# Kernel optimization log

Hardware: AMD Instinct MI355X
Metric: run time of the kernel (lower is better)

## Reference

```python
import jax, jax.numpy as jnp
import numpy as np

B = 256          # batch
H = 1024         # conditioning_size (dec_hid_dim)
D = 256          # gst_dim
G = 32           # num_gst
C = 16           # num_cells
O = 256          # output_size


def setup_inputs() -> dict:
    key = jax.random.key(0)
    ks = jax.random.split(key, 7)
    hidden = jax.random.normal(ks[0], (B, H), dtype=jnp.float32)
    # per-cell embedding tables: nn.Embedding(num_gst, gst_dim) stacked over cells
    gst_emb = jax.random.normal(ks[1], (C, G, D), dtype=jnp.float32)
    # per-cell Linear(gst_dim + cond, cond): weight [H, H + D] (torch [out, in]), bias [H]
    attn_w = jax.random.normal(ks[2], (C, H, H + D), dtype=jnp.float32) * 0.02
    attn_b = jax.random.normal(ks[3], (C, H), dtype=jnp.float32) * 0.02
    # per-cell v: Parameter(torch.rand(cond))
    v = jax.random.uniform(ks[4], (C, H), dtype=jnp.float32)
    # out Linear(gst_dim, output_size)
    out_w = jax.random.normal(ks[5], (O, D), dtype=jnp.float32) * 0.02
    out_b = jax.random.normal(ks[6], (O,), dtype=jnp.float32) * 0.02
    return {"hidden": hidden, "gst_emb": gst_emb, "attn_w": attn_w,
            "attn_b": attn_b, "v": v, "out_w": out_w, "out_b": out_b}


def reference(hidden, gst_emb, attn_w, attn_b, v, out_w, out_b):
    # Original concatenates (hidden, encoder_outputs) along features; split the
    # linear weight accordingly instead of materializing the concat.
    w_hid = attn_w[:, :, :H]        # [C, H, H]
    w_enc = attn_w[:, :, H:]        # [C, H, D]
    # embedding lookup of arange(G) == the table rows themselves (same for all batch)
    enc = gst_emb                   # [C, G, D]
    hid_part = jnp.einsum('bh,coh->bco', hidden, w_hid)     # [B, C, Ho]
    enc_part = jnp.einsum('cgd,cod->cgo', enc, w_enc)       # [C, G, Ho]
    energy = jnp.tanh(hid_part[:, :, None, :] + enc_part[None]
                      + attn_b[None, :, None, :])           # [B, C, G, Ho]
    scores = jnp.einsum('bcgh,ch->bcg', energy, v)          # [B, C, G]
    attention = jax.nn.softmax(scores, axis=-1)             # softmax over num_gst
    weighted = jnp.einsum('bcg,cgd->bcd', attention, enc)   # [B, C, D]
    att_cat = attention.reshape(B, C * G)                   # torch.cat(att_list, dim=1)
    pooled = jnp.mean(weighted, axis=1)                     # [B, D]
    out = pooled @ out_w.T + out_b                          # [B, O]
    return (att_cat, out)
```

## Files before the change

### kernel.cpp

```cpp
#include <hip/hip_runtime.h>
#include <hip/hip_bf16.h>

#define B_  256
#define H_  1024
#define D_  256
#define G_  32
#define C_  16
#define O_  256
#define HD_ 1280
#define N1_ 16384
#define RS_ 40

typedef __attribute__((ext_vector_type(8)))  short short8;
typedef __attribute__((ext_vector_type(4)))  short s16x4;
typedef __attribute__((ext_vector_type(4)))  float f32x4;
typedef __attribute__((ext_vector_type(16))) float f32x16;

#define MFMA32(a, b, c) __builtin_amdgcn_mfma_f32_32x32x16_bf16((a), (b), (c), 0, 0, 0)

__device__ __forceinline__ float tanh_c(float x) {
    float y = __expf(2.f * x);
    float t = 1.f - 2.f * __builtin_amdgcn_rcpf(y + 1.f);
    return fminf(fmaxf(t, -0.99999994f), 0.99999994f);
}

__device__ __forceinline__ short bfhi(float x) {
    return (short)(__float_as_uint(x) >> 16);
}
__device__ __forceinline__ short bflo(float x) {
    float fhi = __uint_as_float(__float_as_uint(x) & 0xFFFF0000u);
    return (short)(__float_as_uint(x - fhi) >> 16);
}

__device__ __forceinline__ void split4(const float4 v, s16x4& hi, s16x4& lo) {
    hi[0] = bfhi(v.x); lo[0] = bflo(v.x);
    hi[1] = bfhi(v.y); lo[1] = bflo(v.y);
    hi[2] = bfhi(v.z); lo[2] = bflo(v.z);
    hi[3] = bfhi(v.w); lo[3] = bflo(v.w);
}

__global__ __launch_bounds__(256, 2) void gemm1_kernel(
    const short* __restrict__ hidH, const short* __restrict__ hidL,
    const float* __restrict__ attn_w, const float* __restrict__ attn_b,
    float* __restrict__ hp)
{
    __shared__ short BsH[2][32 * RS_];
    __shared__ short BsL[2][32 * RS_];

    const int tid  = threadIdx.x;
    const int wave = tid >> 6, lane = tid & 63;
    const int n0  = blockIdx.x * 32;
    const int l31 = lane & 31;
    const int kh  = (lane >> 5) * 8;

    f32x16 acc0, acc1;
    #pragma unroll
    for (int i = 0; i < 16; ++i) { acc0[i] = 0.f; acc1[i] = 0.f; }

    const int rB = tid >> 3, cB = (tid & 7) * 4;
    const float* pB = attn_w + (size_t)(n0 + rB) * HD_ + cB;
    const int wB = rB * RS_ + cB;
    const int boff = l31 * RS_ + kh;

    const size_t aBase = (size_t)(wave * 2) * 32768 + (size_t)lane * 8;
    const short* pH0 = hidH + aBase;
    const short* pH1 = hidH + aBase + 32768;
    const short* pL0 = hidL + aBase;
    const short* pL1 = hidL + aBase + 32768;

    float4 rb[2];
    short8 aH0[2][2], aH1[2][2], aL0[2][2], aL1[2][2];

    rb[0] = *(const float4*)(pB);
    {   s16x4 h_, l_; split4(rb[0], h_, l_);
        *(s16x4*)(&BsH[0][wB]) = h_;
        *(s16x4*)(&BsL[0][wB]) = l_; }
    rb[1] = *(const float4*)(pB + 32);
    aH0[0][0] = *(const short8*)(pH0);
    aH0[0][1] = *(const short8*)(pH0 + 512);
    aH1[0][0] = *(const short8*)(pH1);
    aH1[0][1] = *(const short8*)(pH1 + 512);
    aL0[0][0] = *(const short8*)(pL0);
    aL0[0][1] = *(const short8*)(pL0 + 512);
    aL1[0][0] = *(const short8*)(pL1);
    aL1[0][1] = *(const short8*)(pL1 + 512);
    asm volatile("s_waitcnt lgkmcnt(0)" ::: "memory");
    __builtin_amdgcn_s_barrier();

#define BODY(P, K0, DOW, DOLB, DOLA, DOB)                                     \
    {                                                                         \
        if (DOW) {                                                            \
            s16x4 h_, l_;                                                     \
            split4(rb[P ^ 1], h_, l_);                                        \
            *(s16x4*)(&BsH[P ^ 1][wB]) = h_;                                  \
            *(s16x4*)(&BsL[P ^ 1][wB]) = l_;                                  \
        }                                                                     \
        if (DOLB) rb[P] = *(const float4*)(pB + ((K0) + 2) * 32);             \
        if (DOLA) {                                                           \
            aH0[P ^ 1][0] = *(const short8*)(pH0 + ((K0) + 1) * 1024);        \
            aH0[P ^ 1][1] = *(const short8*)(pH0 + ((K0) + 1) * 1024 + 512);  \
            aH1[P ^ 1][0] = *(const short8*)(pH1 + ((K0) + 1) * 1024);        \
            aH1[P ^ 1][1] = *(const short8*)(pH1 + ((K0) + 1) * 1024 + 512);  \
            aL0[P ^ 1][0] = *(const short8*)(pL0 + ((K0) + 1) * 1024);        \
            aL0[P ^ 1][1] = *(const short8*)(pL0 + ((K0) + 1) * 1024 + 512);  \
            aL1[P ^ 1][0] = *(const short8*)(pL1 + ((K0) + 1) * 1024);        \
            aL1[P ^ 1][1] = *(const short8*)(pL1 + ((K0) + 1) * 1024 + 512);  \
        }                                                                     \
        {                                                                     \
            short8 bh0 = *(const short8*)(&BsH[P][boff]);                     \
            short8 bl0 = *(const short8*)(&BsL[P][boff]);                     \
            short8 bh1 = *(const short8*)(&BsH[P][boff + 16]);                \
            short8 bl1 = *(const short8*)(&BsL[P][boff + 16]);                \
            __builtin_amdgcn_s_setprio(1);                                    \
            acc0 = MFMA32(aH0[P][0], bh0, acc0);                              \
            acc1 = MFMA32(aH1[P][0], bh0, acc1);                              \
            acc0 = MFMA32(aL0[P][0], bh0, acc0);                              \
            acc1 = MFMA32(aL1[P][0], bh0, acc1);                              \
            acc0 = MFMA32(aH0[P][0], bl0, acc0);                              \
            acc1 = MFMA32(aH1[P][0], bl0, acc1);                              \
            acc0 = MFMA32(aH0[P][1], bh1, acc0);                              \
            acc1 = MFMA32(aH1[P][1], bh1, acc1);                              \
            acc0 = MFMA32(aL0[P][1], bh1, acc0);                              \
            acc1 = MFMA32(aL1[P][1], bh1, acc1);                              \
            acc0 = MFMA32(aH0[P][1], bl1, acc0);                              \
            acc1 = MFMA32(aH1[P][1], bl1, acc1);                              \
            __builtin_amdgcn_s_setprio(0);                                    \
        }                                                                     \
        if (DOB) {                                                            \
            asm volatile("s_waitcnt lgkmcnt(0)" ::: "memory");                \
            __builtin_amdgcn_s_barrier();                                     \
        }                                                                     \
    }

    for (int k0 = 0; k0 < 30; k0 += 2) {
        BODY(0, k0, 1, 1, 1, 1)
        BODY(1, k0 + 1, 1, 1, 1, 1)
    }
    BODY(0, 30, 1, 0, 1, 1)
    BODY(1, 31, 0, 0, 0, 0)
#undef BODY

    const int col  = n0 + l31;
    const float bias = attn_b[col];
    const int rbase = wave * 64 + (lane >> 5) * 4;
    float* dcol = hp + col;
    #pragma unroll
    for (int r = 0; r < 16; ++r) {
        const int row = rbase + (r & 3) + 8 * (r >> 2);
        dcol[(size_t)row * N1_]        = tanh_c(acc0[r] + bias);
        dcol[(size_t)(row + 32) * N1_] = tanh_c(acc1[r] + bias);
    }
}

__global__ __launch_bounds__(256) void gemm2_kernel(
    const float* __restrict__ enc, const float* __restrict__ attn_w,
    const float* __restrict__ hidden, float* __restrict__ ep,
    short* __restrict__ hidH, short* __restrict__ hidL)
{
    const int tid  = threadIdx.x;
    const int wave = tid >> 6, lane = tid & 63;

    {
        const int bid = blockIdx.y * 16 + blockIdx.x;
        const int gid = bid * 256 + tid;
        if (gid < 32768) {
            const int s   = gid >> 12;
            const int k0  = (gid >> 7) & 31;
            const int ks  = (gid >> 6) & 1;
            const int ln  = gid & 63;
            const int row = s * 32 + (ln & 31);
            const int colk = k0 * 32 + ks * 16 + (ln >> 5) * 8;
            const float* src = hidden + (size_t)row * H_ + colk;
            s16x4 h0, l0, h1, l1;
            split4(*(const float4*)src, h0, l0);
            split4(*(const float4*)(src + 4), h1, l1);
            *(short8*)(hidH + (size_t)gid * 8) =
                short8{h0[0],h0[1],h0[2],h0[3],h1[0],h1[1],h1[2],h1[3]};
            *(short8*)(hidL + (size_t)gid * 8) =
                short8{l0[0],l0[1],l0[2],l0[3],l1[0],l1[1],l1[2],l1[3]};
        }
    }

    const int c  = blockIdx.y;
    const int n0 = blockIdx.x * 64 + wave * 16;
    const int l16 = lane & 15;
    const int lk  = (lane >> 4) * 8;

#define MFMA16(a, b, c) __builtin_amdgcn_mfma_f32_16x16x32_bf16((a), (b), (c), 0, 0, 0)
    f32x4 acc[2];
    acc[0] = f32x4{0.f, 0.f, 0.f, 0.f};
    acc[1] = f32x4{0.f, 0.f, 0.f, 0.f};

    const float* encp = enc + c * (G_ * D_);
    const float* wp   = attn_w + (size_t)c * H_ * HD_ + H_;

    #pragma unroll
    for (int kk = 0; kk < 8; ++kk) {
        const int k0 = kk * 32 + lk;
        short8 ah[2], al[2], bh, bl;
        #pragma unroll
        for (int mi = 0; mi < 2; ++mi) {
            const float* p = encp + (mi * 16 + l16) * D_ + k0;
            s16x4 h0, l0, h1, l1;
            split4(*(const float4*)p, h0, l0);
            split4(*(const float4*)(p + 4), h1, l1);
            ah[mi] = short8{h0[0],h0[1],h0[2],h0[3],h1[0],h1[1],h1[2],h1[3]};
            al[mi] = short8{l0[0],l0[1],l0[2],l0[3],l1[0],l1[1],l1[2],l1[3]};
        }
        {
            const float* p = wp + (size_t)(n0 + l16) * HD_ + k0;
            s16x4 h0, l0, h1, l1;
            split4(*(const float4*)p, h0, l0);
            split4(*(const float4*)(p + 4), h1, l1);
            bh = short8{h0[0],h0[1],h0[2],h0[3],h1[0],h1[1],h1[2],h1[3]};
            bl = short8{l0[0],l0[1],l0[2],l0[3],l1[0],l1[1],l1[2],l1[3]};
        }
        #pragma unroll
        for (int mi = 0; mi < 2; ++mi) {
            acc[mi] = MFMA16(ah[mi], bh, acc[mi]);
            acc[mi] = MFMA16(al[mi], bh, acc[mi]);
            acc[mi] = MFMA16(ah[mi], bl, acc[mi]);
        }
    }

    const int lr = (lane >> 4) * 4;
    #pragma unroll
    for (int mi = 0; mi < 2; ++mi) {
        const int g = mi * 16 + lr;
        const int o = n0 + l16;
        float* dst = ep + (c * G_ + g) * H_ + o;
        f32x4 vacc = acc[mi];
        dst[0]      = tanh_c(vacc[0]);
        dst[H_]     = tanh_c(vacc[1]);
        dst[2 * H_] = tanh_c(vacc[2]);
        dst[3 * H_] = tanh_c(vacc[3]);
    }
#undef MFMA16
}

__global__ __launch_bounds__(256) void attn_kernel(
    const float* __restrict__ hp, const float* __restrict__ ep,
    const float* __restrict__ v, const float* __restrict__ enc,
    float* __restrict__ out, float* __restrict__ wt)
{
    const int c  = blockIdx.x;
    const int b0 = blockIdx.y * 4;
    const int tid  = threadIdx.x;
    const int wave = tid >> 6, lane = tid & 63;

    __shared__ float s_att[4][G_];
    __shared__ float s_sc[4][G_];

    f32x4 vv[4], tav[4][4];
    const float* vrow = v + c * H_;
    #pragma unroll
    for (int j = 0; j < 4; ++j)
        vv[j] = *(const f32x4*)(vrow + lane * 4 + j * 256);
    #pragma unroll
    for (int bi = 0; bi < 4; ++bi) {
        const float* hprow = hp + (size_t)(b0 + bi) * N1_ + c * H_;
        #pragma unroll
        for (int j = 0; j < 4; ++j)
            tav[bi][j] = *(const f32x4*)(hprow + lane * 4 + j * 256);
    }

    #pragma unroll
    for (int gg = 0; gg < 8; ++gg) {
        const int g = wave * 8 + gg;
        const float* eprow = ep + (size_t)(c * G_ + g) * H_;
        float s[4] = {0.f, 0.f, 0.f, 0.f};
        #pragma unroll
        for (int j = 0; j < 4; ++j) {
            const f32x4 tb = *(const f32x4*)(eprow + lane * 4 + j * 256);
            #pragma unroll
            for (int e = 0; e < 4; ++e) {
                const float tbx = tb[e];
                const float w   = vv[j][e];
                #pragma unroll
                for (int bi = 0; bi < 4; ++bi) {
                    const float ta  = tav[bi][j][e];
                    const float num = ta + tbx;
                    const float den = fmaf(ta, tbx, 1.f);
                    s[bi] = fmaf(num * __builtin_amdgcn_rcpf(den), w, s[bi]);
                }
            }
        }
        #pragma unroll
        for (int off = 32; off > 0; off >>= 1) {
            s[0] += __shfl_down(s[0], off, 64);
            s[1] += __shfl_down(s[1], off, 64);
            s[2] += __shfl_down(s[2], off, 64);
            s[3] += __shfl_down(s[3], off, 64);
        }
        if (lane == 0) {
            s_sc[0][g] = s[0]; s_sc[1][g] = s[1];
            s_sc[2][g] = s[2]; s_sc[3][g] = s[3];
        }
    }
    __syncthreads();

    if (tid < 128) {
        const int bi = tid >> 5, g = tid & 31;
        float sv = s_sc[bi][g];
        float m = sv;
        #pragma unroll
        for (int off = 16; off > 0; off >>= 1)
            m = fmaxf(m, __shfl_xor(m, off, 32));
        const float e = __expf(sv - m);
        float sum = e;
        #pragma unroll
        for (int off = 16; off > 0; off >>= 1)
            sum += __shfl_xor(sum, off, 32);
        const float a = e / sum;
        s_att[bi][g] = a;
        out[(size_t)(b0 + bi) * (C_ * G_) + c * G_ + g] = a;
    }
    __syncthreads();

    float w0 = 0.f, w1 = 0.f, w2 = 0.f, w3 = 0.f;
    const float* encc = enc + c * (G_ * D_) + tid;
    #pragma unroll
    for (int g = 0; g < G_; ++g) {
        const float e = encc[g * D_];
        w0 = fmaf(s_att[0][g], e, w0);
        w1 = fmaf(s_att[1][g], e, w1);
        w2 = fmaf(s_att[2][g], e, w2);
        w3 = fmaf(s_att[3][g], e, w3);
    }
    wt[(size_t)((b0 + 0) * C_ + c) * D_ + tid] = w0;
    wt[(size_t)((b0 + 1) * C_ + c) * D_ + tid] = w1;
    wt[(size_t)((b0 + 2) * C_ + c) * D_ + tid] = w2;
    wt[(size_t)((b0 + 3) * C_ + c) * D_ + tid] = w3;
}

__global__ __launch_bounds__(256) void out_kernel(
    const float* __restrict__ wt, const float* __restrict__ out_w,
    const float* __restrict__ out_b, float* __restrict__ out)
{
    const int b = blockIdx.x, tid = threadIdx.x;
    __shared__ float pooled[D_];

    float s = 0.f;
    #pragma unroll
    for (int c = 0; c < C_; ++c)
        s += wt[(size_t)(b * C_ + c) * D_ + tid];
    pooled[tid] = s * (1.f / 16.f);
    __syncthreads();

    float acc = out_b[tid];
    const float* wrow = out_w + tid * D_;
    #pragma unroll 8
    for (int dc = 0; dc < 64; ++dc) {
        float4 w4 = *(const float4*)(wrow + dc * 4);
        acc += pooled[dc * 4 + 0] * w4.x;
        acc += pooled[dc * 4 + 1] * w4.y;
        acc += pooled[dc * 4 + 2] * w4.z;
        acc += pooled[dc * 4 + 3] * w4.w;
    }
    out[(size_t)B_ * (C_ * G_) + b * O_ + tid] = acc;
}

extern "C" void kernel_launch(void* const* d_in, const int* in_sizes, int n_in,
                              void* d_out, int out_size, void* d_ws, size_t ws_size,
                              hipStream_t stream) {
    const float* hidden = (const float*)d_in[0];
    const float* enc    = (const float*)d_in[1];
    const float* attn_w = (const float*)d_in[2];
    const float* attn_b = (const float*)d_in[3];
    const float* v      = (const float*)d_in[4];
    const float* out_w  = (const float*)d_in[5];
    const float* out_b  = (const float*)d_in[6];
    float* out = (float*)d_out;

    float* hp = (float*)d_ws;
    float* ep = hp + (size_t)B_ * N1_;
    float* wt = ep + (size_t)C_ * G_ * H_;
    short* hidH = (short*)(wt + (size_t)B_ * C_ * D_);
    short* hidL = hidH + (size_t)B_ * H_;

    gemm2_kernel<<<dim3(16, C_), 256, 0, stream>>>(enc, attn_w, hidden, ep, hidH, hidL);
    gemm1_kernel<<<512, 256, 0, stream>>>(hidH, hidL, attn_w, attn_b, hp);
    attn_kernel<<<dim3(C_, B_ / 4), 256, 0, stream>>>(hp, ep, v, enc, out, wt);
    out_kernel<<<B_, 256, 0, stream>>>(wt, out_w, out_b, out);
}
```

Before: 205.4 us.

## Load GEMM1 weight fragments directly into registers, dropping LDS staging and barriers

The hidden-projection GEMM no longer stages the fp32 attention weights through shared memory with per-step barriers. Each wave now loads its own weight fragment from global memory into registers, splits it into bf16 hi/lo, and uses a three-deep register prefetch pipeline for both operands. The grid is remapped so each block covers 64 output columns and 4 batch slabs, with each wave owning a 32-column by 64-row tile. This removes LDS traffic and synchronisation, but weights are now loaded redundantly by waves that share columns, and register pressure goes up.

```diff
diff --git a/kernel.cpp b/kernel.cpp
--- a/kernel.cpp
+++ b/kernel.cpp
@@ -9,7 +9,6 @@
 #define O_  256
 #define HD_ 1280
 #define N1_ 16384
-#define RS_ 40
 
 typedef __attribute__((ext_vector_type(8)))  short short8;
 typedef __attribute__((ext_vector_type(4)))  short s16x4;
@@ -44,105 +43,101 @@
     const float* __restrict__ attn_w, const float* __restrict__ attn_b,
     float* __restrict__ hp)
 {
-    __shared__ short BsH[2][32 * RS_];
-    __shared__ short BsL[2][32 * RS_];
-
     const int tid  = threadIdx.x;
     const int wave = tid >> 6, lane = tid & 63;
-    const int n0  = blockIdx.x * 32;
     const int l31 = lane & 31;
     const int kh  = (lane >> 5) * 8;
 
+    const int n0 = blockIdx.y * 64 + (wave & 1) * 32;
+    const int s0 = blockIdx.x * 4 + (wave >> 1) * 2;
+
     f32x16 acc0, acc1;
     #pragma unroll
     for (int i = 0; i < 16; ++i) { acc0[i] = 0.f; acc1[i] = 0.f; }
 
-    const int rB = tid >> 3, cB = (tid & 7) * 4;
-    const float* pB = attn_w + (size_t)(n0 + rB) * HD_ + cB;
-    const int wB = rB * RS_ + cB;
-    const int boff = l31 * RS_ + kh;
-
-    const size_t aBase = (size_t)(wave * 2) * 32768 + (size_t)lane * 8;
+    const size_t aBase = (size_t)s0 * 32768 + (size_t)lane * 8;
     const short* pH0 = hidH + aBase;
     const short* pH1 = hidH + aBase + 32768;
     const short* pL0 = hidL + aBase;
     const short* pL1 = hidL + aBase + 32768;
 
-    float4 rb[2];
-    short8 aH0[2][2], aH1[2][2], aL0[2][2], aL1[2][2];
-
-    rb[0] = *(const float4*)(pB);
-    {   s16x4 h_, l_; split4(rb[0], h_, l_);
-        *(s16x4*)(&BsH[0][wB]) = h_;
-        *(s16x4*)(&BsL[0][wB]) = l_; }
-    rb[1] = *(const float4*)(pB + 32);
-    aH0[0][0] = *(const short8*)(pH0);
-    aH0[0][1] = *(const short8*)(pH0 + 512);
-    aH1[0][0] = *(const short8*)(pH1);
-    aH1[0][1] = *(const short8*)(pH1 + 512);
-    aL0[0][0] = *(const short8*)(pL0);
-    aL0[0][1] = *(const short8*)(pL0 + 512);
-    aL1[0][0] = *(const short8*)(pL1);
-    aL1[0][1] = *(const short8*)(pL1 + 512);
-    asm volatile("s_waitcnt lgkmcnt(0)" ::: "memory");
-    __builtin_amdgcn_s_barrier();
-
-#define BODY(P, K0, DOW, DOLB, DOLA, DOB)                                     \
+    const float* pBr = attn_w + (size_t)(n0 + l31) * HD_ + kh;
+
+    short8 aH0[3][2], aH1[3][2], aL0[3][2], aL1[3][2];
+    float4 rb[3][4];
+
+#define LOADA(SET, KS)                                                        \
     {                                                                         \
-        if (DOW) {                                                            \
-            s16x4 h_, l_;                                                     \
-            split4(rb[P ^ 1], h_, l_);                                        \
-            *(s16x4*)(&BsH[P ^ 1][wB]) = h_;                                  \
-            *(s16x4*)(&BsL[P ^ 1][wB]) = l_;                                  \
+        const int o_ = (KS) * 1024;                                           \
+        aH0[SET][0] = *(const short8*)(pH0 + o_);                             \
+        aH0[SET][1] = *(const short8*)(pH0 + o_ + 512);                       \
+        aH1[SET][0] = *(const short8*)(pH1 + o_);                             \
+        aH1[SET][1] = *(const short8*)(pH1 + o_ + 512);                       \
+        aL0[SET][0] = *(const short8*)(pL0 + o_);                             \
+        aL0[SET][1] = *(const short8*)(pL0 + o_ + 512);                       \
+        aL1[SET][0] = *(const short8*)(pL1 + o_);                             \
+        aL1[SET][1] = *(const short8*)(pL1 + o_ + 512);                       \
+    }
+#define LOADB(SET, KS)                                                        \
+    {                                                                         \
+        const float* p_ = pBr + (KS) * 32;                                    \
+        rb[SET][0] = *(const float4*)(p_);                                    \
+        rb[SET][1] = *(const float4*)(p_ + 4);                                \
+        rb[SET][2] = *(const float4*)(p_ + 16);                               \
+        rb[SET][3] = *(const float4*)(p_ + 20);                               \
+    }
+
+    LOADB(0, 0) LOADA(0, 0)
+    LOADB(1, 1) LOADA(1, 1)
+    LOADB(2, 2) LOADA(2, 2)
+
+#define BODY(P, K, DOL)                                                       \
+    {                                                                         \
+        short8 bh0, bl0, bh1, bl1;                                            \
+        {                                                                     \
+            s16x4 h0, l0, h1, l1;                                             \
+            split4(rb[P][0], h0, l0); split4(rb[P][1], h1, l1);               \
+            bh0 = short8{h0[0],h0[1],h0[2],h0[3],h1[0],h1[1],h1[2],h1[3]};    \
+            bl0 = short8{l0[0],l0[1],l0[2],l0[3],l1[0],l1[1],l1[2],l1[3]};    \
+            split4(rb[P][2], h0, l0); split4(rb[P][3], h1, l1);               \
+            bh1 = short8{h0[0],h0[1],h0[2],h0[3],h1[0],h1[1],h1[2],h1[3]};    \
+            bl1 = short8{l0[0],l0[1],l0[2],l0[3],l1[0],l1[1],l1[2],l1[3]};    \
         }                                                                     \
-        if (DOLB) rb[P] = *(const float4*)(pB + ((K0) + 2) * 32);             \
-        if (DOLA) {                                                           \
-            aH0[P ^ 1][0] = *(const short8*)(pH0 + ((K0) + 1) * 1024);        \
-            aH0[P ^ 1][1] = *(const short8*)(pH0 + ((K0) + 1) * 1024 + 512);  \
-            aH1[P ^ 1][0] = *(const short8*)(pH1 + ((K0) + 1) * 1024);        \
-            aH1[P ^ 1][1] = *(const short8*)(pH1 + ((K0) + 1) * 1024 + 512);  \
-            aL0[P ^ 1][0] = *(const short8*)(pL0 + ((K0) + 1) * 1024);        \
-            aL0[P ^ 1][1] = *(const short8*)(pL0 + ((K0) + 1) * 1024 + 512);  \
-            aL1[P ^ 1][0] = *(const short8*)(pL1 + ((K0) + 1) * 1024);        \
-            aL1[P ^ 1][1] = *(const short8*)(pL1 + ((K0) + 1) * 1024 + 512);  \
-        }                                                                     \
-        {                                                                     \
-            short8 bh0 = *(const short8*)(&BsH[P][boff]);                     \
-            short8 bl0 = *(const short8*)(&BsL[P][boff]);                     \
-            short8 bh1 = *(const short8*)(&BsH[P][boff + 16]);                \
-            short8 bl1 = *(const short8*)(&BsL[P][boff + 16]);                \
-            __builtin_amdgcn_s_setprio(1);                                    \
-            acc0 = MFMA32(aH0[P][0], bh0, acc0);                              \
-            acc1 = MFMA32(aH1[P][0], bh0, acc1);                              \
-            acc0 = MFMA32(aL0[P][0], bh0, acc0);                              \
-            acc1 = MFMA32(aL1[P][0], bh0, acc1);                              \
-            acc0 = MFMA32(aH0[P][0], bl0, acc0);                              \
-            acc1 = MFMA32(aH1[P][0], bl0, acc1);                              \
-            acc0 = MFMA32(aH0[P][1], bh1, acc0);                              \
-            acc1 = MFMA32(aH1[P][1], bh1, acc1);                              \
-            acc0 = MFMA32(aL0[P][1], bh1, acc0);                              \
-            acc1 = MFMA32(aL1[P][1], bh1, acc1);                              \
-            acc0 = MFMA32(aH0[P][1], bl1, acc0);                              \
-            acc1 = MFMA32(aH1[P][1], bl1, acc1);                              \
-            __builtin_amdgcn_s_setprio(0);                                    \
-        }                                                                     \
-        if (DOB) {                                                            \
-            asm volatile("s_waitcnt lgkmcnt(0)" ::: "memory");                \
-            __builtin_amdgcn_s_barrier();                                     \
-        }                                                                     \
-    }
-
-    for (int k0 = 0; k0 < 30; k0 += 2) {
-        BODY(0, k0, 1, 1, 1, 1)
-        BODY(1, k0 + 1, 1, 1, 1, 1)
-    }
-    BODY(0, 30, 1, 0, 1, 1)
-    BODY(1, 31, 0, 0, 0, 0)
+        if (DOL) LOADB(P, (K) + 3)                                            \
+        __builtin_amdgcn_s_setprio(1);                                        \
+        acc0 = MFMA32(aH0[P][0], bh0, acc0);                                  \
+        acc1 = MFMA32(aH1[P][0], bh0, acc1);                                  \
+        acc0 = MFMA32(aL0[P][0], bh0, acc0);                                  \
+        acc1 = MFMA32(aL1[P][0], bh0, acc1);                                  \
+        acc0 = MFMA32(aH0[P][0], bl0, acc0);                                  \
+        acc1 = MFMA32(aH1[P][0], bl0, acc1);                                  \
+        acc0 = MFMA32(aH0[P][1], bh1, acc0);                                  \
+        acc1 = MFMA32(aH1[P][1], bh1, acc1);                                  \
+        acc0 = MFMA32(aL0[P][1], bh1, acc0);                                  \
+        acc1 = MFMA32(aL1[P][1], bh1, acc1);                                  \
+        acc0 = MFMA32(aH0[P][1], bl1, acc0);                                  \
+        acc1 = MFMA32(aH1[P][1], bl1, acc1);                                  \
+        __builtin_amdgcn_s_setprio(0);                                        \
+        if (DOL) LOADA(P, (K) + 3)                                            \
+    }
+
+    for (int k = 0; k < 27; k += 3) {
+        BODY(0, k, 1)
+        BODY(1, k + 1, 1)
+        BODY(2, k + 2, 1)
+    }
+    BODY(0, 27, 1)
+    BODY(1, 28, 1)
+    BODY(2, 29, 0)
+    BODY(0, 30, 0)
+    BODY(1, 31, 0)
 #undef BODY
+#undef LOADA
+#undef LOADB
 
     const int col  = n0 + l31;
     const float bias = attn_b[col];
-    const int rbase = wave * 64 + (lane >> 5) * 4;
+    const int rbase = s0 * 32 + (lane >> 5) * 4;
     float* dcol = hp + col;
     #pragma unroll
     for (int r = 0; r < 16; ++r) {
@@ -379,7 +374,7 @@
     short* hidL = hidH + (size_t)B_ * H_;
 
     gemm2_kernel<<<dim3(16, C_), 256, 0, stream>>>(enc, attn_w, hidden, ep, hidH, hidL);
-    gemm1_kernel<<<512, 256, 0, stream>>>(hidH, hidL, attn_w, attn_b, hp);
+    gemm1_kernel<<<dim3(2, 256), 256, 0, stream>>>(hidH, hidL, attn_w, attn_b, hp);
     attn_kernel<<<dim3(C_, B_ / 4), 256, 0, stream>>>(hp, ep, v, enc, out, wt);
     out_kernel<<<B_, 256, 0, stream>>>(wt, out_w, out_b, out);
 }
```

Result: slower. 230.1 us (+12.0%).
